# Kernel tuning notes

Hardware: AMD Instinct MI355X
Metric: run time of the kernel (lower is better)

The kernel has to match this reference:

```python
import jax, jax.numpy as jnp
import numpy as np
from jax import lax

T_NO = 200
SUB_NO = 16
E_NO = 2000
I_NO = 500
T_DATA = 20000
COS_BASIS_NO = 16
COS_SHIFT = 1.0
COS_SCALE = 4.0


def make_cos_basis(T_no):
    # [cos_basis_no, T_no] raised-cosine basis, matches torch loop exactly
    i = jnp.arange(COS_BASIS_NO, dtype=jnp.float32)[:, None]
    phi = (jnp.pi / 2.0) * i
    x = jnp.arange(T_no, dtype=jnp.float32)[None, :]
    raw = COS_SCALE * jnp.log(x + COS_SHIFT)
    basis = 0.5 * jnp.cos(raw - phi) + 0.5
    return jnp.where((raw < phi - jnp.pi) | (raw > phi + jnp.pi), 0.0, basis)


@jax.custom_vjp
def step(x):
    # torch.heaviside(x, 0): 1 for x>0, 0 for x<=0
    return jnp.where(x > 0, 1.0, 0.0).astype(x.dtype)

def _step_fwd(x):
    return step(x), x

def _step_bwd(x, g):
    return (g / (1.0 + jnp.abs(x)) ** 2,)

step.defvjp(_step_fwd, _step_bwd)


def _depthwise_causal(pad, kern_flipped):
    # pad: [T_data+T_no, sub], kern_flipped: [sub, T_no] (already flipped, torch-style)
    lhs = pad.T[None]                      # [1, sub, L]
    rhs = kern_flipped[:, None, :]          # [sub, 1, T_no]
    out = lax.conv_general_dilated(lhs, rhs, (1,), 'VALID',
                                   dimension_numbers=('NCH', 'OIH', 'NCH'),
                                   feature_group_count=SUB_NO)
    return out[0].T                         # [T_data+1, sub]


def _srm_forward(S_e, S_i, C_den, C_syn_e, C_syn_i, Tau_syn_e, Tau_syn_i,
                 W_syn_e, W_syn_i, Delta_syn_e, Delta_syn_i, Tau_spk, W_spk,
                 W_hist, Theta):
    T_no = T_NO
    cos_basis = make_cos_basis(T_no)
    syn_e = S_e @ C_syn_e.T                 # [T_data, sub]
    syn_i = S_i @ C_syn_i.T

    t = jnp.arange(T_no, dtype=jnp.float32)[None, :]
    t_e = jnp.maximum(t - jnp.exp(Delta_syn_e)[:, None], 0.0)
    t_i = jnp.maximum(t - jnp.exp(Delta_syn_i)[:, None], 0.0)
    tt_e = t_e / jnp.exp(Tau_syn_e)[:, None]
    tt_i = t_i / jnp.exp(Tau_syn_i)[:, None]
    e_kern = tt_e * jnp.exp(-tt_e) * jnp.exp(W_syn_e)[:, None]       # [sub, T_no]
    i_kern = -tt_i * jnp.exp(-tt_i) * jnp.exp(W_syn_i)[:, None]

    zpad = jnp.zeros((T_no, SUB_NO), syn_e.dtype)
    filt_e = _depthwise_causal(jnp.concatenate([zpad, syn_e], 0), jnp.flip(e_kern, 1))[:-1]
    filt_i = _depthwise_causal(jnp.concatenate([zpad, syn_i], 0), jnp.flip(i_kern, 1))[:-1]
    syn = filt_e + filt_i                   # [T_data, sub]

    tt_spk = t / jnp.exp(Tau_spk)[:, None]
    spk_kern = tt_spk * jnp.exp(-tt_spk) * jnp.exp(W_spk)[:, None]   # [sub, T_no]
    hist_kern = W_hist @ cos_basis                                    # [sub, T_no]
    spk_kern_f = jnp.flip(spk_kern, 1)
    hist_kern_f = jnp.flip(hist_kern, 1)

    def step_fn(buf, syn_t):
        # buf: [T_no, sub] rolling spike history, buf[-1] = most recent
        hist_in = jnp.einsum('ts,st->s', buf, hist_kern_f)
        spk_in_raw = jnp.einsum('ts,st->s', buf, spk_kern_f)
        spk_in = C_den @ spk_in_raw
        sub_in = hist_in + spk_in + syn_t + Theta
        s = step(sub_in)
        return jnp.concatenate([buf[1:], s[None]], 0), s

    buf0 = jnp.zeros((T_no, SUB_NO), syn.dtype)
    _, spk_out = lax.scan(step_fn, buf0, syn)   # [T_data, sub]

    out_filters = jnp.vstack([e_kern, i_kern, spk_kern, hist_kern])  # [4*sub, T_no]
    return spk_out, out_filters


def setup_inputs() -> dict:
    key = jax.random.key(0)
    ks = jax.random.split(key, 10)
    # sparse-ish spike trains
    S_e = (jax.random.uniform(ks[0], (T_DATA, E_NO)) < 0.02).astype(jnp.float32)
    S_i = (jax.random.uniform(ks[1], (T_DATA, I_NO)) < 0.02).astype(jnp.float32)
    # each synapse maps to exactly one subunit
    C_syn_e = jax.nn.one_hot(jax.random.randint(ks[2], (E_NO,), 0, SUB_NO), SUB_NO).T.astype(jnp.float32)
    C_syn_i = jax.nn.one_hot(jax.random.randint(ks[3], (I_NO,), 0, SUB_NO), SUB_NO).T.astype(jnp.float32)
    C_den = (jax.random.uniform(ks[4], (SUB_NO, SUB_NO)) < 0.15).astype(jnp.float32)
    ones = jnp.ones(SUB_NO, jnp.float32)
    return {
        'S_e': S_e, 'S_i': S_i, 'C_den': C_den, 'C_syn_e': C_syn_e, 'C_syn_i': C_syn_i,
        'Tau_syn_e': ones * 1.0, 'Tau_syn_i': ones * 1.0,
        'W_syn_e': ones * 0.5, 'W_syn_i': ones * 0.5,
        'Delta_syn_e': ones * 1.0, 'Delta_syn_i': ones * 1.0,
        'Tau_spk': ones * 1.0, 'W_spk': ones * -1.0,
        'W_hist': 0.1 * jax.random.normal(ks[5], (SUB_NO, COS_BASIS_NO), jnp.float32),
        'Theta': -0.5 * ones + 0.1 * jax.random.normal(ks[6], (SUB_NO,), jnp.float32),
    }


def reference(S_e, S_i, C_den, C_syn_e, C_syn_i, Tau_syn_e, Tau_syn_i, W_syn_e,
              W_syn_i, Delta_syn_e, Delta_syn_i, Tau_spk, W_spk, W_hist, Theta):
    return _srm_forward(S_e, S_i, C_den, C_syn_e, C_syn_i, Tau_syn_e, Tau_syn_i,
                        W_syn_e, W_syn_i, Delta_syn_e, Delta_syn_i, Tau_spk, W_spk,
                        W_hist, Theta)
```

## Files before the change

### kernel.cpp

```cpp
#include <hip/hip_runtime.h>

#ifndef M_PI
#define M_PI 3.14159265358979323846
#endif

#define T_DATA 20000
#define E_NO_C 2000
#define I_NO_C 500
#define SUB 16
#define TNO 200
#define NGRP 5000
#define NSUP 2500

typedef float v2f __attribute__((ext_vector_type(2)));

template <bool B> struct BC { static constexpr bool v = B; };

__device__ __forceinline__ float quad_sum(float v) {
  int a = __builtin_amdgcn_mov_dpp(__float_as_int(v), 177, 0xf, 0xf, true);
  v += __int_as_float(a);
  int b = __builtin_amdgcn_mov_dpp(__float_as_int(v), 78, 0xf, 0xf, true);
  v += __int_as_float(b);
  return v;
}

__device__ __forceinline__ void bar_sync() {
  asm volatile("s_waitcnt lgkmcnt(0)" ::: "memory");
  __builtin_amdgcn_s_barrier();
  asm volatile("" ::: "memory");
}

__global__ void filters_k(const float* __restrict__ Tau_e, const float* __restrict__ Tau_i,
                          const float* __restrict__ W_e,  const float* __restrict__ W_i,
                          const float* __restrict__ D_e,  const float* __restrict__ D_i,
                          const float* __restrict__ Tau_spk, const float* __restrict__ W_spk,
                          const float* __restrict__ W_hist,
                          float* __restrict__ filt_out) {
  int id = blockIdx.x * blockDim.x + threadIdx.x;
  if (id >= 64 * TNO) return;
  int r = id / TNO, x = id % TNO;
  int s = r & 15, kind = r >> 4;
  double xd = (double)x;
  double val;
  if (kind == 0) {
    double te = xd - exp((double)D_e[s]); te = te > 0.0 ? te : 0.0;
    double tt = te / exp((double)Tau_e[s]);
    val = tt * exp(-tt) * exp((double)W_e[s]);
  } else if (kind == 1) {
    double ti = xd - exp((double)D_i[s]); ti = ti > 0.0 ? ti : 0.0;
    double tt = ti / exp((double)Tau_i[s]);
    val = -tt * exp(-tt) * exp((double)W_i[s]);
  } else if (kind == 2) {
    double tt = xd / exp((double)Tau_spk[s]);
    val = tt * exp(-tt) * exp((double)W_spk[s]);
  } else {
    double raw = 4.0 * log(xd + 1.0);
    double acc = 0.0;
    for (int i = 0; i < 16; ++i) {
      double phi = (M_PI / 2.0) * (double)i;
      double b = (raw < phi - M_PI || raw > phi + M_PI) ? 0.0
                                                        : (0.5 * cos(raw - phi) + 0.5);
      acc += (double)W_hist[s * 16 + i] * b;
    }
    val = acc;
  }
  filt_out[id] = (float)val;
}

#define ETILE 500
__global__ __launch_bounds__(256) void synmm_k(const float* __restrict__ S,
                                               const float* __restrict__ C,
                                               float* __restrict__ out, int E) {
  __shared__ __align__(16) float Cs[16][ETILE];
  int tid = threadIdx.x;
  int s = tid & 15, tt = tid >> 4;
  long t = (long)blockIdx.x * 16 + tt;
  const float* Srow = S + t * E;
  float acc = 0.f;
  for (int tb = 0; tb < E; tb += ETILE) {
    __syncthreads();
    for (int i = tid; i < 16 * ETILE; i += 256) {
      int s2 = i / ETILE, k2 = i - s2 * ETILE;
      Cs[s2][k2] = C[(long)s2 * E + tb + k2];
    }
    __syncthreads();
    const float* Crow = &Cs[s][0];
    const float* Sp = Srow + tb;
#pragma unroll 2
    for (int e = 0; e < ETILE; e += 4) {
      float4 a = *(const float4*)(Sp + e);
      float4 c = *(const float4*)(Crow + e);
      acc = fmaf(a.x, c.x, acc); acc = fmaf(a.y, c.y, acc);
      acc = fmaf(a.z, c.z, acc); acc = fmaf(a.w, c.w, acc);
    }
  }
  out[t * 16 + s] = acc;
}

__global__ void conv_k(const float* __restrict__ syn_e, const float* __restrict__ syn_i,
                       const float* __restrict__ filt, const float* __restrict__ Theta,
                       float* __restrict__ synTh) {
  __shared__ float ek[16][201];
  __shared__ float ik[16][201];
  int tid = threadIdx.x;
  for (int idx = tid; idx < 16 * TNO; idx += 256) {
    ek[idx / TNO][idx % TNO] = filt[idx];
    ik[idx / TNO][idx % TNO] = filt[16 * TNO + idx];
  }
  __syncthreads();
  int s = tid & 15, tt = tid >> 4;
  int t = blockIdx.x * 16 + tt;
  float acc = Theta[s];
  if (t >= TNO) {
#pragma unroll 4
    for (int j = 0; j < TNO; ++j) {
      int u = t - 1 - j;
      acc += ek[s][j] * syn_e[u * 16 + s] + ik[s][j] * syn_i[u * 16 + s];
    }
  } else {
    for (int j = 0; j < t; ++j) {
      int u = t - 1 - j;
      acc += ek[s][j] * syn_e[u * 16 + s] + ik[s][j] * syn_i[u * 16 + s];
    }
  }
  synTh[t * 16 + s] = acc;
}

__global__ __launch_bounds__(448, 1) void scan13_k(const float* __restrict__ synTh,
                                                   const float* __restrict__ filt,
                                                   const float* __restrict__ C_den,
                                                   const float* __restrict__ Tau_spk,
                                                   const float* __restrict__ W_spk,
                                                   float* __restrict__ spk_out) {
  __shared__ __align__(16) float ring[16][452];
  __shared__ __align__(16) float oPartF[2][5][2][64];
  __shared__ __align__(16) float farsumF[2][2][64];
  __shared__ __align__(16) float synStage[2][4][16][20];
  const int tid = threadIdx.x;
  const int widx = tid >> 6;
  const int l = tid & 63;
  const int s = l & 15, q = l >> 4;

  for (int i = tid; i < 16 * 452; i += 448) (&ring[0][0])[i] = 0.f;
  for (int i = tid; i < 2 * 5 * 2 * 64; i += 448) (&oPartF[0][0][0][0])[i] = 0.f;
  for (int i = tid; i < 2 * 2 * 64; i += 448) (&farsumF[0][0][0])[i] = 0.f;
  __syncthreads();
  if (widx == 4) {
    int e0 = 4 * l;
    float4 v = *(const float4*)&synTh[e0];
    int t0 = e0 >> 4, s0 = e0 & 15;
    int g = t0 >> 2, K = t0 & 3;
    synStage[0][g & 3][s0 + 0][K] = v.x;
    synStage[0][g & 3][s0 + 1][K] = v.y;
    synStage[0][g & 3][s0 + 2][K] = v.z;
    synStage[0][g & 3][s0 + 3][K] = v.w;
  }
  __syncthreads();

  if (widx == 0) {
    const float* hrow = filt + (48 + s) * TNO;
    float hk[15];
#pragma unroll
    for (int i = 0; i < 15; ++i) hk[i] = hrow[i];

    float t0v = Tau_spk[0], w0v = W_spk[0];
    bool okrow = (Tau_spk[s] == t0v) && (W_spk[s] == w0v);
    unsigned cd = 0u;
#pragma unroll
    for (int j = 0; j < 16; ++j) {
      float cv = C_den[s * 16 + j];
      okrow = okrow && (cv == 0.f || cv == 1.f);
      cd |= (cv != 0.f) ? (1u << j) : 0u;
    }
    const bool uni = (bool)__all((int)okrow);

    const double tau  = exp((double)Tau_spk[s]);
    const double aa   = exp(-1.0 / tau);
    const double c2a  = exp((double)W_spk[s]) * aa / tau;
    const double twoa = 2.0 * aa;
    const double na2  = -aa * aa;

    double twoa4[4], na24[4], c2a4[4], yd0a[4], yd1a[4];
    float cden4[4];
#pragma unroll
    for (int r = 0; r < 4; ++r) {
      int j = 4 * q + r;
      double tj = exp((double)Tau_spk[j]);
      double aj = exp(-1.0 / tj);
      twoa4[r] = 2.0 * aj; na24[r] = -aj * aj;
      c2a4[r]  = exp((double)W_spk[j]) * aj / tj;
      yd0a[r] = 0.0; yd1a[r] = 0.0;
      cden4[r] = C_den[s * 16 + j];
    }

    double zA = 0.0, zB = 0.0;
    float mixu = 0.f, mix1 = 0.f;
    float sgPrev = 0.f;
    float S0 = 0.f, S1 = 0.f, S2 = 0.f, S3 = 0.f;
    float cA0 = 0.f, cA1 = 0.f, cA2 = 0.f, cA3 = 0.f;
    float ccA0 = 0.f, ccA1 = 0.f, ccA2 = 0.f, ccA3 = 0.f;
    float nrA0 = 0.f, nrA1 = 0.f, nrA2 = 0.f, nrA3 = 0.f;
    float ccB0 = 0.f, ccB1 = 0.f, ccB2 = 0.f, ccB3 = 0.f;
    float nrB0 = 0.f, nrB1 = 0.f, nrB2 = 0.f, nrB3 = 0.f;

#define STEP(SGD, PRE, SGOUT)                                                 \
    {                                                                         \
      float sub = fmaf(hk[0], (SGD), (PRE));                                  \
      unsigned long long bal = __ballot(sub > 0.f);                           \
      float sg = sub > 0.f ? 1.f : 0.f;                                       \
      if constexpr (UNI) {                                                    \
        unsigned xm = (unsigned)bal & cd;   \
        double zc = fma(twoa, zB, fma(na2, zA, c2a * (double)__popc(xm)));    \
        zA = zB; zB = zc;                                                     \
        mixu = (float)zA;                                                     \
      } else {                                                                \
        unsigned mk = (unsigned)bal & 0xFFFFu;                                \
        float p = 0.f;                                                        \
        _Pragma("unroll")                                                     \
        for (int r = 0; r < 4; ++r) {                                         \
          double xr = (double)((mk >> (4 * q + r)) & 1u);                     \
          double y2 = fma(twoa4[r], yd1a[r], fma(na24[r], yd0a[r], c2a4[r] * xr)); \
          yd0a[r] = yd1a[r]; yd1a[r] = y2;                                    \
          p = fmaf(cden4[r], (float)y2, p);                                   \
        }                                                                     \
        p += __shfl_xor(p, 16); p += __shfl_xor(p, 32);                       \
        float mixn = mix1; mix1 = p;                                          \
        mixu = mixn;                                                          \
      }                                                                       \
      (SGOUT) = sg;                                                           \
    }

    auto scan_loop = [&](auto uc) {
      constexpr bool UNI = decltype(uc)::v;
      for (int M = 0; M < NSUP; ++M) {
        const int gA = 2 * M, gB = 2 * M + 1;
        float4 fsA = *(const float4*)&farsumF[M & 1][0][4 * s];
        float4 fsB = *(const float4*)&farsumF[M & 1][1][4 * s];
        float4 synA = *(const float4*)&synStage[(gA >> 2) & 1][gA & 3][s][0];
        float4 synB = *(const float4*)&synStage[(gB >> 2) & 1][gB & 3][s][0];

        float ocA0 = ((nrA0 + fsA.x) + (synA.x + cA0)) + ccA0;
        float ocA1 = ((nrA1 + fsA.y) + (synA.y + cA1)) + ccA1;
        float ocA2 = ((nrA2 + fsA.z) + (synA.z + cA2)) + ccA2;
        float ocA3 = ((nrA3 + fsA.w) + (synA.w + cA3)) + ccA3;

        float SA0, SA1, SA2, SA3;
        STEP(sgPrev, ocA0 + mixu, SA0)
        float pend2 = hk[1] * SA0;
        float pend3 = hk[2] * SA0;
        STEP(SA0, ocA1 + mixu, SA1)
        pend3 = fmaf(hk[1], SA1, pend3);
        STEP(SA1, (ocA2 + mixu) + pend2, SA2)
        STEP(SA2, (ocA3 + mixu) + pend3, SA3)

        if (l < 16) {
          int u = (8 * M) & 255;
          float4 w0; w0.x = SA0; w0.y = SA1; w0.z = SA2; w0.w = SA3;
          *(float4*)&ring[s][u] = w0;
          if (u < 192) *(float4*)&ring[s][u + 256] = w0;
        }

        float cB0 = fmaf(hk[1], SA2, fmaf(hk[2], SA1, hk[3] * SA0));
        float cB1 = fmaf(hk[1], SA3, fmaf(hk[2], SA2, fmaf(hk[3], SA1, hk[4] * SA0)));
        float cB2 = fmaf(hk[2], SA3, fmaf(hk[3], SA2, fmaf(hk[4], SA1, hk[5] * SA0)));
        float cB3 = fmaf(hk[3], SA3, fmaf(hk[4], SA2, fmaf(hk[5], SA1, hk[6] * SA0)));

        float ocB0 = ((nrB0 + fsB.x) + (synB.x + cB0)) + ccB0;
        float ocB1 = ((nrB1 + fsB.y) + (synB.y + cB1)) + ccB1;
        float ocB2 = ((nrB2 + fsB.z) + (synB.z + cB2)) + ccB2;
        float ocB3 = ((nrB3 + fsB.w) + (synB.w + cB3)) + ccB3;

        float SB0, SB1, SB2, SB3;
        STEP(SA3, ocB0 + mixu, SB0)
        float pend2b = hk[1] * SB0;
        float pend3b = hk[2] * SB0;
        STEP(SB0, ocB1 + mixu, SB1)
        pend3b = fmaf(hk[1], SB1, pend3b);
        STEP(SB1, (ocB2 + mixu) + pend2b, SB2)
        STEP(SB2, (ocB3 + mixu) + pend3b, SB3)

        if (l < 16) {
          int u = (8 * M + 4) & 255;
          float4 w0; w0.x = SB0; w0.y = SB1; w0.z = SB2; w0.w = SB3;
          *(float4*)&ring[s][u] = w0;
          if (u < 192) *(float4*)&ring[s][u + 256] = w0;
        }

        cA0 = fmaf(hk[1], SB2, fmaf(hk[2], SB1, hk[3] * SB0));
        cA1 = fmaf(hk[1], SB3, fmaf(hk[2], SB2, fmaf(hk[3], SB1, hk[4] * SB0)));
        cA2 = fmaf(hk[2], SB3, fmaf(hk[3], SB2, fmaf(hk[4], SB1, hk[5] * SB0)));
        cA3 = fmaf(hk[3], SB3, fmaf(hk[4], SB2, fmaf(hk[5], SB1, hk[6] * SB0)));
        ccA0 = fmaf(hk[7], SA0, fmaf(hk[6], SA1, fmaf(hk[5], SA2, hk[4] * SA3)));
        ccA1 = fmaf(hk[8], SA0, fmaf(hk[7], SA1, fmaf(hk[6], SA2, hk[5] * SA3)));
        ccA2 = fmaf(hk[9], SA0, fmaf(hk[8], SA1, fmaf(hk[7], SA2, hk[6] * SA3)));
        ccA3 = fmaf(hk[10], SA0, fmaf(hk[9], SA1, fmaf(hk[8], SA2, hk[7] * SA3)));
        ccB0 = fmaf(hk[7], SB0, fmaf(hk[6], SB1, fmaf(hk[5], SB2, hk[4] * SB3)));
        ccB1 = fmaf(hk[8], SB0, fmaf(hk[7], SB1, fmaf(hk[6], SB2, hk[5] * SB3)));
        ccB2 = fmaf(hk[9], SB0, fmaf(hk[8], SB1, fmaf(hk[7], SB2, hk[6] * SB3)));
        ccB3 = fmaf(hk[10], SB0, fmaf(hk[9], SB1, fmaf(hk[8], SB2, hk[7] * SB3)));
        nrA0 = fmaf(hk[11], S0, fmaf(hk[10], S1, fmaf(hk[9], S2, hk[8] * S3)));
        nrA1 = fmaf(hk[12], S0, fmaf(hk[11], S1, fmaf(hk[10], S2, hk[9] * S3)));
        nrA2 = fmaf(hk[13], S0, fmaf(hk[12], S1, fmaf(hk[11], S2, hk[10] * S3)));
        nrA3 = fmaf(hk[14], S0, fmaf(hk[13], S1, fmaf(hk[12], S2, hk[11] * S3)));
        nrB0 = fmaf(hk[11], SA0, fmaf(hk[10], SA1, fmaf(hk[9], SA2, hk[8] * SA3)));
        nrB1 = fmaf(hk[12], SA0, fmaf(hk[11], SA1, fmaf(hk[10], SA2, hk[9] * SA3)));
        nrB2 = fmaf(hk[13], SA0, fmaf(hk[12], SA1, fmaf(hk[11], SA2, hk[10] * SA3)));
        nrB3 = fmaf(hk[14], SA0, fmaf(hk[13], SA1, fmaf(hk[12], SA2, hk[11] * SA3)));

        S0 = SB0; S1 = SB1; S2 = SB2; S3 = SB3;
        sgPrev = SB3;
        bar_sync();
      }
    };
    if (uni) scan_loop(BC<true>{});
    else     scan_loop(BC<false>{});
#undef STEP
  } else if (widx == 4) {
    const int s2 = l >> 2, K = l & 3;
    const float* hrow = filt + (48 + s2) * TNO;
    float hc5[32];
#pragma unroll
    for (int x = 0; x < 32; ++x) hc5[x] = hrow[12 + K + x];

    for (int M = 0; M < NSUP; ++M) {
      float4 vv;
      const bool doStage = (M & 1) && (2 * M + 2 < NGRP);
      if (doStage) vv = *(const float4*)&synTh[(2 * M + 2) * 64 + 4 * l];

      int pos0 = (8 * M - 36) & 255;
      const float4* rp = (const float4*)&ring[s2][pos0];
      float e[36];
#pragma unroll
      for (int i = 0; i < 9; ++i) {
        float4 R = rp[i];
        e[4 * i + 0] = R.x; e[4 * i + 1] = R.y; e[4 * i + 2] = R.z; e[4 * i + 3] = R.w;
      }
      float f5v[2];
#pragma unroll
      for (int p = 0; p < 2; ++p) {
        float o0c, o1c, o2c, o3c;
        {
          float oo[4];
#pragma unroll
          for (int c = 0; c < 4; ++c) {
            v2f p01, p23, p45, p67, PR7, PR5, PR3, PR1;
            int ofs = 4 * p + 8 * c;
            p01.x = e[ofs + 0]; p01.y = e[ofs + 1];
            p23.x = e[ofs + 2]; p23.y = e[ofs + 3];
            p45.x = e[ofs + 4]; p45.y = e[ofs + 5];
            p67.x = e[ofs + 6]; p67.y = e[ofs + 7];
            PR7.x = hc5[31 - 8 * c]; PR7.y = hc5[30 - 8 * c];
            PR5.x = hc5[29 - 8 * c]; PR5.y = hc5[28 - 8 * c];
            PR3.x = hc5[27 - 8 * c]; PR3.y = hc5[26 - 8 * c];
            PR1.x = hc5[25 - 8 * c]; PR1.y = hc5[24 - 8 * c];
            v2f a = PR7 * p01; a += PR5 * p23; a += PR3 * p45; a += PR1 * p67;
            oo[c] = a.x + a.y;
          }
          o0c = oo[0]; o1c = oo[1]; o2c = oo[2]; o3c = oo[3];
        }
        f5v[p] = (o0c + o1c) + (o2c + o3c);
      }

      const int slot = M & 1, wbuf = (M + 1) & 1;
      float t0e = oPartF[slot][0][0][l] + oPartF[slot][1][0][l];
      float t1e = oPartF[slot][2][0][l] + oPartF[slot][3][0][l];
      float t2e = oPartF[slot][4][0][l] + f5v[0];
      farsumF[wbuf][0][l] = (t0e + t1e) + t2e;
      float t0o = oPartF[slot][0][1][l] + oPartF[slot][1][1][l];
      float t1o = oPartF[slot][2][1][l] + oPartF[slot][3][1][l];
      float t2o = oPartF[slot][4][1][l] + f5v[1];
      farsumF[wbuf][1][l] = (t0o + t1o) + t2o;

      if (doStage) {
        int e0 = (2 * M + 2) * 64 + 4 * l;
        int t0i = e0 >> 4, s0 = e0 & 15;
        int g = t0i >> 2, Kk = t0i & 3;
        int buf = (g >> 2) & 1;
        synStage[buf][g & 3][s0 + 0][Kk] = vv.x;
        synStage[buf][g & 3][s0 + 1][Kk] = vv.y;
        synStage[buf][g & 3][s0 + 2][Kk] = vv.z;
        synStage[buf][g & 3][s0 + 3][Kk] = vv.w;
      }
      if ((M & 3) == 0 && M > 0) {
        int n = 2 * M;
        int We = (4 * n - 1) & 255;
        if (We < 191) We += 256;
        int base2 = We - 31;
#pragma unroll
        for (int r = 0; r < 2; ++r) {
          int eo = 64 * (n - 8) + 256 * r + 4 * l;
          int t0i = eo >> 4, s0 = eo & 15;
          int pos = base2 + (t0i - 4 * (n - 8));
          float4 w;
          w.x = ring[s0 + 0][pos]; w.y = ring[s0 + 1][pos];
          w.z = ring[s0 + 2][pos]; w.w = ring[s0 + 3][pos];
          *(float4*)&spk_out[eo] = w;
        }
      }
      bar_sync();
    }
    {
      int n = NGRP;
      int We = (4 * n - 1) & 255;
      if (We < 191) We += 256;
      int base2 = We - 31;
#pragma unroll
      for (int r = 0; r < 2; ++r) {
        int eo = 64 * (n - 8) + 256 * r + 4 * l;
        int t0i = eo >> 4, s0 = eo & 15;
        int pos = base2 + (t0i - 4 * (n - 8));
        float4 w;
        w.x = ring[s0 + 0][pos]; w.y = ring[s0 + 1][pos];
        w.z = ring[s0 + 2][pos]; w.w = ring[s0 + 3][pos];
        *(float4*)&spk_out[eo] = w;
      }
    }
  } else {
    const int f = (widx < 4) ? (widx - 1) : (widx - 2);
    const int s2 = l >> 2, qq = l & 3;
    const float* hrow = filt + (48 + s2) * TNO;
    const int base = 196 - 32 * f - 8 * qq;
    float ca[11];
#pragma unroll
    for (int m = 0; m < 11; ++m) {
      int hidx = base + m;
      ca[m] = (hidx <= 199) ? hrow[hidx] : 0.f;
    }
    v2f pr[11];
    pr[0].x = 0.f; pr[0].y = 0.f;
#pragma unroll
    for (int m = 1; m < 11; ++m) { pr[m].x = ca[m]; pr[m].y = ca[m - 1]; }

    for (int M = 0; M < NSUP; ++M) {
      int W0 = (8 * M - 188 + 32 * f + 8 * qq) & 255;
      const float4* rp = (const float4*)&ring[s2][W0];
      float4 V0 = rp[0], V1 = rp[1], V2 = rp[2];
      v2f p01, p23, p45, p67, q01, q23, q45, q67;
      p01.x = V0.x; p01.y = V0.y; p23.x = V0.z; p23.y = V0.w;
      p45.x = V1.x; p45.y = V1.y; p67.x = V1.z; p67.y = V1.w;
      q01.x = V1.x; q01.y = V1.y; q23.x = V1.z; q23.y = V1.w;
      q45.x = V2.x; q45.y = V2.y; q67.x = V2.z; q67.y = V2.w;
      float o0, o1, o2, o3, o4, o5, o6, o7;
      { v2f a = pr[7] * p01;  a += pr[5] * p23; a += pr[3] * p45; a += pr[1] * p67; o0 = a.x + a.y; }
      { v2f a = pr[8] * p01;  a += pr[6] * p23; a += pr[4] * p45; a += pr[2] * p67; o1 = a.x + a.y; }
      { v2f a = pr[9] * p01;  a += pr[7] * p23; a += pr[5] * p45; a += pr[3] * p67; o2 = a.x + a.y; }
      { v2f a = pr[10] * p01; a += pr[8] * p23; a += pr[6] * p45; a += pr[4] * p67; o3 = a.x + a.y; }
      { v2f a = pr[7] * q01;  a += pr[5] * q23; a += pr[3] * q45; a += pr[1] * q67; o4 = a.x + a.y; }
      { v2f a = pr[8] * q01;  a += pr[6] * q23; a += pr[4] * q45; a += pr[2] * q67; o5 = a.x + a.y; }
      { v2f a = pr[9] * q01;  a += pr[7] * q23; a += pr[5] * q45; a += pr[3] * q67; o6 = a.x + a.y; }
      { v2f a = pr[10] * q01; a += pr[8] * q23; a += pr[6] * q45; a += pr[4] * q67; o7 = a.x + a.y; }
      o0 = quad_sum(o0); o1 = quad_sum(o1); o2 = quad_sum(o2); o3 = quad_sum(o3);
      o4 = quad_sum(o4); o5 = quad_sum(o5); o6 = quad_sum(o6); o7 = quad_sum(o7);
      float myoE = (qq == 0) ? o0 : (qq == 1) ? o1 : (qq == 2) ? o2 : o3;
      float myoO = (qq == 0) ? o4 : (qq == 1) ? o5 : (qq == 2) ? o6 : o7;
      const int slot = (M + 1) & 1;
      oPartF[slot][f][0][l] = myoE;
      oPartF[slot][f][1][l] = myoO;
      bar_sync();
    }
  }
}

extern "C" void kernel_launch(void* const* d_in, const int* in_sizes, int n_in,
                              void* d_out, int out_size, void* d_ws, size_t ws_size,
                              hipStream_t stream) {
  const float* S_e     = (const float*)d_in[0];
  const float* S_i     = (const float*)d_in[1];
  const float* C_den   = (const float*)d_in[2];
  const float* C_syn_e = (const float*)d_in[3];
  const float* C_syn_i = (const float*)d_in[4];
  const float* Tau_e   = (const float*)d_in[5];
  const float* Tau_i   = (const float*)d_in[6];
  const float* W_e     = (const float*)d_in[7];
  const float* W_i     = (const float*)d_in[8];
  const float* D_e     = (const float*)d_in[9];
  const float* D_i     = (const float*)d_in[10];
  const float* Tau_spk = (const float*)d_in[11];
  const float* W_spk   = (const float*)d_in[12];
  const float* W_hist  = (const float*)d_in[13];
  const float* Theta   = (const float*)d_in[14];

  float* out     = (float*)d_out;
  float* spk_out = out;
  float* filt    = out + 320000;

  float* ws    = (float*)d_ws;
  float* syn_e = ws;
  float* syn_i = ws + 320000;
  float* synTh = ws + 640000;

  filters_k<<<50, 256, 0, stream>>>(Tau_e, Tau_i, W_e, W_i, D_e, D_i,
                                    Tau_spk, W_spk, W_hist, filt);
  synmm_k<<<1250, 256, 0, stream>>>(S_e, C_syn_e, syn_e, E_NO_C);
  synmm_k<<<1250, 256, 0, stream>>>(S_i, C_syn_i, syn_i, I_NO_C);
  conv_k<<<1250, 256, 0, stream>>>(syn_e, syn_i, filt, Theta, synTh);
  scan13_k<<<1, 448, 0, stream>>>(synTh, filt, C_den, Tau_spk, W_spk, spk_out);
}
```

Before: 2.008 ms.

## Split scan iteration into two barrier phases and prefetch next operands mid-step

The single-block scan kernel grows from 448 to 512 threads and now uses two barriers per super-step instead of one. The serial scan wave loads the next iteration's farsum and synaptic inputs right after the first barrier, so the shared-memory reads come off the critical dependency chain. Wave 4 becomes an idle wave that only joins barriers, and the staging role moves to wave 7. The cost is an extra barrier per iteration across eight waves, which may outweigh the hidden load latency.

```diff
diff --git a/kernel.cpp b/kernel.cpp
--- a/kernel.cpp
+++ b/kernel.cpp
@@ -126,7 +126,7 @@
   synTh[t * 16 + s] = acc;
 }
 
-__global__ __launch_bounds__(448, 1) void scan13_k(const float* __restrict__ synTh,
+__global__ __launch_bounds__(512, 1) void scan15_k(const float* __restrict__ synTh,
                                                    const float* __restrict__ filt,
                                                    const float* __restrict__ C_den,
                                                    const float* __restrict__ Tau_spk,
@@ -141,11 +141,11 @@
   const int l = tid & 63;
   const int s = l & 15, q = l >> 4;
 
-  for (int i = tid; i < 16 * 452; i += 448) (&ring[0][0])[i] = 0.f;
-  for (int i = tid; i < 2 * 5 * 2 * 64; i += 448) (&oPartF[0][0][0][0])[i] = 0.f;
-  for (int i = tid; i < 2 * 2 * 64; i += 448) (&farsumF[0][0][0])[i] = 0.f;
+  for (int i = tid; i < 16 * 452; i += 512) (&ring[0][0])[i] = 0.f;
+  for (int i = tid; i < 2 * 5 * 2 * 64; i += 512) (&oPartF[0][0][0][0])[i] = 0.f;
+  for (int i = tid; i < 2 * 2 * 64; i += 512) (&farsumF[0][0][0])[i] = 0.f;
   __syncthreads();
-  if (widx == 4) {
+  if (widx == 7) {
     int e0 = 4 * l;
     float4 v = *(const float4*)&synTh[e0];
     int t0 = e0 >> 4, s0 = e0 & 15;
@@ -203,13 +203,18 @@
     float ccB0 = 0.f, ccB1 = 0.f, ccB2 = 0.f, ccB3 = 0.f;
     float nrB0 = 0.f, nrB1 = 0.f, nrB2 = 0.f, nrB3 = 0.f;
 
+    float4 fsA_r = *(const float4*)&farsumF[0][0][4 * s];
+    float4 fsB_r = *(const float4*)&farsumF[0][1][4 * s];
+    float4 synA_r = *(const float4*)&synStage[0][0][s][0];
+    float4 synB_r = *(const float4*)&synStage[0][1][s][0];
+
 #define STEP(SGD, PRE, SGOUT)                                                 \
     {                                                                         \
       float sub = fmaf(hk[0], (SGD), (PRE));                                  \
       unsigned long long bal = __ballot(sub > 0.f);                           \
       float sg = sub > 0.f ? 1.f : 0.f;                                       \
       if constexpr (UNI) {                                                    \
-        unsigned xm = (unsigned)bal & cd;   \
+        unsigned xm = (unsigned)bal & cd;              \
         double zc = fma(twoa, zB, fma(na2, zA, c2a * (double)__popc(xm)));    \
         zA = zB; zB = zc;                                                     \
         mixu = (float)zA;                                                     \
@@ -233,16 +238,10 @@
     auto scan_loop = [&](auto uc) {
       constexpr bool UNI = decltype(uc)::v;
       for (int M = 0; M < NSUP; ++M) {
-        const int gA = 2 * M, gB = 2 * M + 1;
-        float4 fsA = *(const float4*)&farsumF[M & 1][0][4 * s];
-        float4 fsB = *(const float4*)&farsumF[M & 1][1][4 * s];
-        float4 synA = *(const float4*)&synStage[(gA >> 2) & 1][gA & 3][s][0];
-        float4 synB = *(const float4*)&synStage[(gB >> 2) & 1][gB & 3][s][0];
-
-        float ocA0 = ((nrA0 + fsA.x) + (synA.x + cA0)) + ccA0;
-        float ocA1 = ((nrA1 + fsA.y) + (synA.y + cA1)) + ccA1;
-        float ocA2 = ((nrA2 + fsA.z) + (synA.z + cA2)) + ccA2;
-        float ocA3 = ((nrA3 + fsA.w) + (synA.w + cA3)) + ccA3;
+        float ocA0 = ((nrA0 + fsA_r.x) + (synA_r.x + cA0)) + ccA0;
+        float ocA1 = ((nrA1 + fsA_r.y) + (synA_r.y + cA1)) + ccA1;
+        float ocA2 = ((nrA2 + fsA_r.z) + (synA_r.z + cA2)) + ccA2;
+        float ocA3 = ((nrA3 + fsA_r.w) + (synA_r.w + cA3)) + ccA3;
 
         float SA0, SA1, SA2, SA3;
         STEP(sgPrev, ocA0 + mixu, SA0)
@@ -265,10 +264,10 @@
         float cB2 = fmaf(hk[2], SA3, fmaf(hk[3], SA2, fmaf(hk[4], SA1, hk[5] * SA0)));
         float cB3 = fmaf(hk[3], SA3, fmaf(hk[4], SA2, fmaf(hk[5], SA1, hk[6] * SA0)));
 
-        float ocB0 = ((nrB0 + fsB.x) + (synB.x + cB0)) + ccB0;
-        float ocB1 = ((nrB1 + fsB.y) + (synB.y + cB1)) + ccB1;
-        float ocB2 = ((nrB2 + fsB.z) + (synB.z + cB2)) + ccB2;
-        float ocB3 = ((nrB3 + fsB.w) + (synB.w + cB3)) + ccB3;
+        float ocB0 = ((nrB0 + fsB_r.x) + (synB_r.x + cB0)) + ccB0;
+        float ocB1 = ((nrB1 + fsB_r.y) + (synB_r.y + cB1)) + ccB1;
+        float ocB2 = ((nrB2 + fsB_r.z) + (synB_r.z + cB2)) + ccB2;
+        float ocB3 = ((nrB3 + fsB_r.w) + (synB_r.w + cB3)) + ccB3;
 
         float SB0, SB1, SB2, SB3;
         STEP(SA3, ocB0 + mixu, SB0)
@@ -284,6 +283,17 @@
           float4 w0; w0.x = SB0; w0.y = SB1; w0.z = SB2; w0.w = SB3;
           *(float4*)&ring[s][u] = w0;
           if (u < 192) *(float4*)&ring[s][u + 256] = w0;
+        }
+
+        bar_sync();
+
+        {
+          const int Mn = M + 1;
+          const int gAn = 2 * Mn, gBn = 2 * Mn + 1;
+          fsA_r = *(const float4*)&farsumF[Mn & 1][0][4 * s];
+          fsB_r = *(const float4*)&farsumF[Mn & 1][1][4 * s];
+          synA_r = *(const float4*)&synStage[(gAn >> 2) & 1][gAn & 3][s][0];
+          synB_r = *(const float4*)&synStage[(gBn >> 2) & 1][gBn & 3][s][0];
         }
 
         cA0 = fmaf(hk[1], SB2, fmaf(hk[2], SB1, hk[3] * SB0));
@@ -316,6 +326,11 @@
     else     scan_loop(BC<false>{});
 #undef STEP
   } else if (widx == 4) {
+    for (int M = 0; M < NSUP; ++M) {
+      bar_sync();
+      bar_sync();
+    }
+  } else if (widx == 7) {
     const int s2 = l >> 2, K = l & 3;
     const float* hrow = filt + (48 + s2) * TNO;
     float hc5[32];
@@ -338,27 +353,23 @@
       float f5v[2];
 #pragma unroll
       for (int p = 0; p < 2; ++p) {
-        float o0c, o1c, o2c, o3c;
-        {
-          float oo[4];
-#pragma unroll
-          for (int c = 0; c < 4; ++c) {
-            v2f p01, p23, p45, p67, PR7, PR5, PR3, PR1;
-            int ofs = 4 * p + 8 * c;
-            p01.x = e[ofs + 0]; p01.y = e[ofs + 1];
-            p23.x = e[ofs + 2]; p23.y = e[ofs + 3];
-            p45.x = e[ofs + 4]; p45.y = e[ofs + 5];
-            p67.x = e[ofs + 6]; p67.y = e[ofs + 7];
-            PR7.x = hc5[31 - 8 * c]; PR7.y = hc5[30 - 8 * c];
-            PR5.x = hc5[29 - 8 * c]; PR5.y = hc5[28 - 8 * c];
-            PR3.x = hc5[27 - 8 * c]; PR3.y = hc5[26 - 8 * c];
-            PR1.x = hc5[25 - 8 * c]; PR1.y = hc5[24 - 8 * c];
-            v2f a = PR7 * p01; a += PR5 * p23; a += PR3 * p45; a += PR1 * p67;
-            oo[c] = a.x + a.y;
-          }
-          o0c = oo[0]; o1c = oo[1]; o2c = oo[2]; o3c = oo[3];
+        float oo[4];
+#pragma unroll
+        for (int c = 0; c < 4; ++c) {
+          v2f p01, p23, p45, p67, PR7, PR5, PR3, PR1;
+          int ofs = 4 * p + 8 * c;
+          p01.x = e[ofs + 0]; p01.y = e[ofs + 1];
+          p23.x = e[ofs + 2]; p23.y = e[ofs + 3];
+          p45.x = e[ofs + 4]; p45.y = e[ofs + 5];
+          p67.x = e[ofs + 6]; p67.y = e[ofs + 7];
+          PR7.x = hc5[31 - 8 * c]; PR7.y = hc5[30 - 8 * c];
+          PR5.x = hc5[29 - 8 * c]; PR5.y = hc5[28 - 8 * c];
+          PR3.x = hc5[27 - 8 * c]; PR3.y = hc5[26 - 8 * c];
+          PR1.x = hc5[25 - 8 * c]; PR1.y = hc5[24 - 8 * c];
+          v2f a = PR7 * p01; a += PR5 * p23; a += PR3 * p45; a += PR1 * p67;
+          oo[c] = a.x + a.y;
         }
-        f5v[p] = (o0c + o1c) + (o2c + o3c);
+        f5v[p] = (oo[0] + oo[1]) + (oo[2] + oo[3]);
       }
 
       const int slot = M & 1, wbuf = (M + 1) & 1;
@@ -381,6 +392,9 @@
         synStage[buf][g & 3][s0 + 2][Kk] = vv.z;
         synStage[buf][g & 3][s0 + 3][Kk] = vv.w;
       }
+
+      bar_sync();
+
       if ((M & 3) == 0 && M > 0) {
         int n = 2 * M;
         int We = (4 * n - 1) & 255;
@@ -457,6 +471,7 @@
       oPartF[slot][f][0][l] = myoE;
       oPartF[slot][f][1][l] = myoO;
       bar_sync();
+      bar_sync();
     }
   }
 }
@@ -494,5 +509,5 @@
   synmm_k<<<1250, 256, 0, stream>>>(S_e, C_syn_e, syn_e, E_NO_C);
   synmm_k<<<1250, 256, 0, stream>>>(S_i, C_syn_i, syn_i, I_NO_C);
   conv_k<<<1250, 256, 0, stream>>>(syn_e, syn_i, filt, Theta, synTh);
-  scan13_k<<<1, 448, 0, stream>>>(synTh, filt, C_den, Tau_spk, W_spk, spk_out);
-}
+  scan15_k<<<1, 512, 0, stream>>>(synTh, filt, C_den, Tau_spk, W_spk, spk_out);
+}
```

Result: faster. 1.924 ms (-4.2%).
